# Optimization experiments

Hardware: AMD Instinct MI355X
Metric: run time of the kernel (lower is better)

Reference implementation:

```python
import jax, jax.numpy as jnp
import numpy as np

GN_GROUPS = 32
GN_EPS = 1e-5


def _conv3x3(x, w, b):
    # NCHW 3x3 conv, stride 1, pad 1
    y = jax.lax.conv_general_dilated(x, w, (1, 1), [(1, 1), (1, 1)],
                                     dimension_numbers=('NCHW', 'OIHW', 'NCHW'))
    return y + b[None, :, None, None]


def _bilinear(x, py, px):
    # x: [N,C,H,W]; py,px: [N,H,W] fractional sample coords; zeros outside.
    N, C, H, W = x.shape
    y0 = jnp.floor(py)
    x0 = jnp.floor(px)
    wy = py - y0
    wx = px - x0
    xf = x.reshape(N, C, H * W)
    out = jnp.zeros((N, C, H, W), x.dtype)
    corners = ((y0, x0, (1 - wy) * (1 - wx)),
               (y0, x0 + 1, (1 - wy) * wx),
               (y0 + 1, x0, wy * (1 - wx)),
               (y0 + 1, x0 + 1, wy * wx))
    for yy, xx, w in corners:
        valid = ((yy >= 0) & (yy <= H - 1) & (xx >= 0) & (xx <= W - 1)).astype(x.dtype)
        yi = jnp.clip(yy, 0, H - 1).astype(jnp.int32)
        xi = jnp.clip(xx, 0, W - 1).astype(jnp.int32)
        idx = (yi * W + xi).reshape(N, 1, H * W)
        g = jnp.take_along_axis(xf, idx, axis=2).reshape(N, C, H, W)
        out = out + g * (w * valid)[:, None]
    return out


def setup_inputs() -> dict:
    key = jax.random.key(0)
    ks = jax.random.split(key, 8)
    N, C, H, W = 4, 128, 160, 160
    s = 0.05
    return {
        'x': jax.random.normal(ks[0], (N, C, H, W), jnp.float32),
        'w_tm': jax.random.normal(ks[1], (4, C, 3, 3), jnp.float32) * s,
        'b_tm': jax.random.normal(ks[2], (4,), jnp.float32) * s,
        'w_tr': jax.random.normal(ks[3], (2, C, 3, 3), jnp.float32) * s,
        'b_tr': jax.random.normal(ks[4], (2,), jnp.float32) * s,
        'w_dcn': jax.random.normal(ks[5], (C, C, 3, 3), jnp.float32) * s,
        'gn_gamma': jnp.ones((C,), jnp.float32),
        'gn_beta': jnp.zeros((C,), jnp.float32),
    }


def reference(x, w_tm, b_tm, w_tr, b_tr, w_dcn, gn_gamma, gn_beta):
    N, C, H, W = x.shape
    Cout = w_dcn.shape[0]
    # regular 3x3 grid offsets: row0 = ky, row1 = kx, k ordered ky-major
    R = jnp.array([[-1., -1., -1., 0., 0., 0., 1., 1., 1.],
                   [-1., 0., 1., -1., 0., 1., -1., 0., 1.]], x.dtype)
    tm = _conv3x3(x, w_tm, b_tm)   # [N,4,H,W] -> per-pixel 2x2 affine
    tr = _conv3x3(x, w_tr, b_tr)   # [N,2,H,W] -> per-pixel (dy,dx) translation
    tmm = tm.transpose(0, 2, 3, 1).reshape(N, H, W, 2, 2)
    off = jnp.einsum('nhwij,jk->nhwik', tmm, R) - R  # [N,H,W,2,9]
    dy = off[:, :, :, 0, :] + tr[:, 0][..., None]    # [N,H,W,9]
    dx = off[:, :, :, 1, :] + tr[:, 1][..., None]
    hh = jnp.arange(H, dtype=x.dtype)[None, :, None, None]
    ww = jnp.arange(W, dtype=x.dtype)[None, None, :, None]
    kk = jnp.arange(9)
    ky = (kk // 3).astype(x.dtype)
    kx = (kk % 3).astype(x.dtype)
    py = hh - 1.0 + ky + dy  # stride=1, pad=1, dilation=1
    px = ww - 1.0 + kx + dx
    wk = w_dcn.reshape(Cout, C, 9)
    out = jnp.zeros((N, Cout, H, W), x.dtype)
    for k in range(9):  # fixed small loop over kernel points
        s = _bilinear(x, py[..., k], px[..., k])
        out = out + jnp.einsum('nchw,oc->nohw', s, wk[:, :, k])
    # GroupNorm
    og = out.reshape(N, GN_GROUPS, (Cout // GN_GROUPS) * H * W)
    mu = og.mean(axis=2, keepdims=True)
    var = og.var(axis=2, keepdims=True)
    og = (og - mu) * jax.lax.rsqrt(var + GN_EPS)
    out = og.reshape(N, Cout, H, W) * gn_gamma[None, :, None, None] + gn_beta[None, :, None, None]
    return jax.nn.relu(out + x)
```

## Files before the change

### kernel.cpp

```cpp
#include <hip/hip_runtime.h>
#include <hip/hip_fp16.h>
#include <math.h>

#define Hh 160
#define Ww 160
#define Cc 128
#define HW 25600
#define NPIX 102400

typedef __attribute__((ext_vector_type(8))) _Float16 half8;
typedef __attribute__((ext_vector_type(4))) float f32x4;
typedef __attribute__((ext_vector_type(4))) unsigned int u32x4;

union h2u { __half2 h; unsigned int u; };

#define WS_OFFS 0u
#define WS_WA   7372800u
#define WS_GSUM 7667712u
#define WS_GSQ  7668224u
#define WS_XT   7668736u
#define WS_RAW  33883136u

__global__ void wtrans_kernel(const float* __restrict__ w_dcn,
                              unsigned short* __restrict__ wA) {
    int idx = blockIdx.x * 256 + threadIdx.x;
    if (idx >= 9 * 128 * 128) return;
    int k = idx >> 14;
    int o = (idx >> 7) & 127;
    int c = idx & 127;
    wA[idx] = __half_as_ushort(__float2half(w_dcn[(o * 128 + c) * 9 + k]));
}

__global__ void __launch_bounds__(256) xpose_kernel(
    const float* __restrict__ x, unsigned short* __restrict__ xT) {
    __shared__ float L[128 * 65];
    int b = blockIdx.x;
    int n = b / 400;
    int px0 = (b - n * 400) * 64;
    int t = threadIdx.x;
    const float* xn = x + (size_t)n * Cc * HW + px0;
#pragma unroll
    for (int i = 0; i < 32; ++i) {
        int idx = i * 256 + t;
        int ch = idx >> 6;
        int pxl = idx & 63;
        L[ch * 65 + pxl] = xn[(size_t)ch * HW + pxl];
    }
    __syncthreads();
    unsigned short* dst = xT + ((size_t)n * HW + px0) * 128;
#pragma unroll
    for (int j = 0; j < 16; ++j) {
        int idx = j * 256 + t;
        int pxl = idx >> 6;
        int cp = idx & 63;
        h2u cv;
        cv.h = __floats2half2_rn(L[(2 * cp) * 65 + pxl],
                                 L[(2 * cp + 1) * 65 + pxl]);
        *(unsigned int*)(dst + (size_t)pxl * 128 + cp * 2) = cv.u;
    }
}

__global__ void __launch_bounds__(256) offs_kernel(
    const float* __restrict__ x, const float* __restrict__ w_tm,
    const float* __restrict__ b_tm, const float* __restrict__ w_tr,
    const float* __restrict__ b_tr, float* __restrict__ offs2) {
    __shared__ float wt[128 * 9 * 8];
    int t = threadIdx.x;
    for (int idx = t; idx < 6912; idx += 256) {
        int j = idx % 6;
        int rest = idx / 6;
        int tap = rest % 9;
        int c = rest / 9;
        float v = (j < 4) ? w_tm[(j * 128 + c) * 9 + tap]
                          : w_tr[((j - 4) * 128 + c) * 9 + tap];
        wt[rest * 8 + j] = v;
    }
    __syncthreads();
    int bid = blockIdx.x;
    int blk = (bid & 7) * 50 + (bid >> 3);
    int p = blk * 256 + t;
    int n = p / HW;
    int hw = p - n * HW;
    int h = hw / Ww;
    int w = hw - h * Ww;
    int addr[9];
    float msk[9];
#pragma unroll
    for (int tap = 0; tap < 9; ++tap) {
        int dy = tap / 3 - 1, dx = tap % 3 - 1;
        int yy = h + dy, xx = w + dx;
        bool v = (yy >= 0) && (yy < Hh) && (xx >= 0) && (xx < Ww);
        addr[tap] = v ? yy * Ww + xx : 0;
        msk[tap] = v ? 1.f : 0.f;
    }
    float a0 = 0, a1 = 0, a2 = 0, a3 = 0, a4 = 0, a5 = 0;
    const float* xn = x + n * Cc * HW;
#pragma unroll 2
    for (int c = 0; c < Cc; ++c) {
        const float* xc = xn + c * HW;
#pragma unroll
        for (int tap = 0; tap < 9; ++tap) {
            float v = msk[tap] * xc[addr[tap]];
            const float* wp = &wt[(c * 9 + tap) * 8];
            float4 w4 = *(const float4*)wp;
            float2 w2 = *(const float2*)(wp + 4);
            a0 += v * w4.x; a1 += v * w4.y; a2 += v * w4.z; a3 += v * w4.w;
            a4 += v * w2.x; a5 += v * w2.y;
        }
    }
    a0 += b_tm[0]; a1 += b_tm[1]; a2 += b_tm[2]; a3 += b_tm[3];
    a4 += b_tr[0]; a5 += b_tr[1];
#pragma unroll
    for (int k = 0; k < 9; ++k) {
        float r0 = (float)(k / 3) - 1.f;
        float r1 = (float)(k % 3) - 1.f;
        float2 st;
        st.x = (float)h + a0 * r0 + a1 * r1 + a4;
        st.y = (float)w + a2 * r0 + a3 * r1 + a5;
        *(float2*)(offs2 + ((size_t)k * NPIX + p) * 2) = st;
    }
}

__global__ void __launch_bounds__(256, 3) dcn2_kernel(
    const unsigned short* __restrict__ xT, const float* __restrict__ offs2,
    const unsigned short* __restrict__ wA, float* __restrict__ raw,
    float* __restrict__ gsum, float* __restrict__ gsq) {
    __shared__ __align__(16) unsigned short Bt[2 * 64 * 128];
    int t = threadIdx.x;
    int lane = t & 63;
    int wid = t >> 6;
    int wm = wid & 1, wn = wid >> 1;
    int quad = lane >> 4, l15 = lane & 15;
    int sub = lane >> 4;
    int s = lane & 15;

    int bid = blockIdx.x;
    int blk = (bid & 7) * 200 + (bid >> 3);
    int px0 = blk * 64;
    int n = px0 / HW;
    int hw0 = px0 - n * HW;
    const unsigned short* xb = xT + (size_t)n * HW * 128;
    const char* Ag = (const char*)wA;
    const float2* offv = (const float2*)offs2;
    int pbase = px0 + wid * 16 + sub;
    int sb = s << 3;

    f32x4 acc[4][2];
#pragma unroll
    for (int i = 0; i < 4; ++i)
#pragma unroll
        for (int j = 0; j < 2; ++j) acc[i][j] = (f32x4)0.f;

    float2 pc[4], pcn[4];
    u32x4 v00[2], v01[2], v10[2], v11[2];
    float w00[2], w01[2], w10[2], w11[2];

#define ISSUE(sl, r) do {                                                   \
    float py_ = pc[r].x, px_ = pc[r].y;                                     \
    float y0f_ = floorf(py_), x0f_ = floorf(px_);                           \
    float fy_ = py_ - y0f_, fx_ = px_ - x0f_;                               \
    int y0_ = (int)y0f_, xi0_ = (int)x0f_;                                  \
    int y1_ = y0_ + 1, xi1_ = xi0_ + 1;                                     \
    float wa_ = (1.f - fy_) * (1.f - fx_), wb_ = (1.f - fy_) * fx_;         \
    float wc_ = fy_ * (1.f - fx_), wd_ = fy_ * fx_;                         \
    bool vy0_ = (unsigned)y0_ < (unsigned)Hh;                               \
    bool vy1_ = (unsigned)y1_ < (unsigned)Hh;                               \
    bool vx0_ = (unsigned)xi0_ < (unsigned)Ww;                              \
    bool vx1_ = (unsigned)xi1_ < (unsigned)Ww;                              \
    w00[sl] = (vy0_ && vx0_) ? wa_ : 0.f;                                   \
    w01[sl] = (vy0_ && vx1_) ? wb_ : 0.f;                                   \
    w10[sl] = (vy1_ && vx0_) ? wc_ : 0.f;                                   \
    w11[sl] = (vy1_ && vx1_) ? wd_ : 0.f;                                   \
    int cy0_ = vy0_ ? y0_ : 0, cy1_ = vy1_ ? y1_ : 0;                       \
    int cx0_ = vx0_ ? xi0_ : 0, cx1_ = vx1_ ? xi1_ : 0;                     \
    v00[sl] = *(const u32x4*)(xb + ((size_t)(cy0_ * Ww + cx0_) << 7) + sb); \
    v01[sl] = *(const u32x4*)(xb + ((size_t)(cy0_ * Ww + cx1_) << 7) + sb); \
    v10[sl] = *(const u32x4*)(xb + ((size_t)(cy1_ * Ww + cx0_) << 7) + sb); \
    v11[sl] = *(const u32x4*)(xb + ((size_t)(cy1_ * Ww + cx1_) << 7) + sb); \
} while (0)

#define COMBINE(sl, r, bufbase) do {                                        \
    int p_ = wid * 16 + (r) * 4 + sub;                                      \
    __half2 W00_ = __float2half2_rn(w00[sl]);                               \
    __half2 W01_ = __float2half2_rn(w01[sl]);                               \
    __half2 W10_ = __float2half2_rn(w10[sl]);                               \
    __half2 W11_ = __float2half2_rn(w11[sl]);                               \
    u32x4 outv_;                                                            \
    _Pragma("unroll")                                                       \
    for (int e = 0; e < 4; ++e) {                                           \
        h2u a_, b_, c_, d_, o_;                                             \
        a_.u = v00[sl][e]; b_.u = v01[sl][e];                               \
        c_.u = v10[sl][e]; d_.u = v11[sl][e];                               \
        __half2 t_ = __hmul2(W11_, d_.h);                                   \
        t_ = __hfma2(W10_, c_.h, t_);                                       \
        t_ = __hfma2(W01_, b_.h, t_);                                       \
        t_ = __hfma2(W00_, a_.h, t_);                                       \
        o_.h = t_;                                                          \
        outv_[e] = o_.u;                                                    \
    }                                                                       \
    *(u32x4*)&Bt[(bufbase) + p_ * 128 + ((s ^ (p_ & 15)) << 3)] = outv_;    \
} while (0)

#define MQUAD(q) do {                                                       \
    half8 a0_, a1_, a2_, a3_, b0_, b1_;                                     \
    a0_ = *(const half8*)(Ag + ((size_t)(k * 128 + wm * 64 + 0 + l15) << 8) \
                          + (q) * 64 + quad * 16);                          \
    a1_ = *(const half8*)(Ag + ((size_t)(k * 128 + wm * 64 + 16 + l15) << 8)\
                          + (q) * 64 + quad * 16);                          \
    a2_ = *(const half8*)(Ag + ((size_t)(k * 128 + wm * 64 + 32 + l15) << 8)\
                          + (q) * 64 + quad * 16);                          \
    a3_ = *(const half8*)(Ag + ((size_t)(k * 128 + wm * 64 + 48 + l15) << 8)\
                          + (q) * 64 + quad * 16);                          \
    {                                                                       \
        int row0_ = wn * 32 + l15;                                          \
        int row1_ = wn * 32 + 16 + l15;                                     \
        int ur0_ = ((q) * 4 + quad) ^ (row0_ & 15);                         \
        int ur1_ = ((q) * 4 + quad) ^ (row1_ & 15);                         \
        b0_ = *(const half8*)&Bt[bufr + row0_ * 128 + ur0_ * 8];            \
        b1_ = *(const half8*)&Bt[bufr + row1_ * 128 + ur1_ * 8];            \
    }                                                                       \
    acc[0][0] = __builtin_amdgcn_mfma_f32_16x16x32_f16(a0_, b0_, acc[0][0], 0, 0, 0); \
    acc[0][1] = __builtin_amdgcn_mfma_f32_16x16x32_f16(a0_, b1_, acc[0][1], 0, 0, 0); \
    acc[1][0] = __builtin_amdgcn_mfma_f32_16x16x32_f16(a1_, b0_, acc[1][0], 0, 0, 0); \
    acc[1][1] = __builtin_amdgcn_mfma_f32_16x16x32_f16(a1_, b1_, acc[1][1], 0, 0, 0); \
    acc[2][0] = __builtin_amdgcn_mfma_f32_16x16x32_f16(a2_, b0_, acc[2][0], 0, 0, 0); \
    acc[2][1] = __builtin_amdgcn_mfma_f32_16x16x32_f16(a2_, b1_, acc[2][1], 0, 0, 0); \
    acc[3][0] = __builtin_amdgcn_mfma_f32_16x16x32_f16(a3_, b0_, acc[3][0], 0, 0, 0); \
    acc[3][1] = __builtin_amdgcn_mfma_f32_16x16x32_f16(a3_, b1_, acc[3][1], 0, 0, 0); \
} while (0)

#pragma unroll
    for (int r = 0; r < 4; ++r) pc[r] = offv[pbase + r * 4];
    ISSUE(0, 0); ISSUE(1, 1);
    COMBINE(0, 0, 0); COMBINE(1, 1, 0);
    ISSUE(0, 2); ISSUE(1, 3);
    COMBINE(0, 2, 0); COMBINE(1, 3, 0);
#pragma unroll
    for (int r = 0; r < 4; ++r) pc[r] = offv[(size_t)1 * NPIX + pbase + r * 4];
    __syncthreads();

    for (int k = 0; k < 9; ++k) {
        int bufr = (k & 1) * (64 * 128);
        int bufw = ((k + 1) & 1) * (64 * 128);
        if (k < 7) {
#pragma unroll
            for (int r = 0; r < 4; ++r)
                pcn[r] = offv[(size_t)(k + 2) * NPIX + pbase + r * 4];
        }
        if (k < 8) { ISSUE(0, 0); ISSUE(1, 1); }
        MQUAD(0); MQUAD(1);
        if (k < 8) {
            COMBINE(0, 0, bufw); COMBINE(1, 1, bufw);
            ISSUE(0, 2); ISSUE(1, 3);
        }
        MQUAD(2); MQUAD(3);
        if (k < 8) { COMBINE(0, 2, bufw); COMBINE(1, 3, bufw); }
        __syncthreads();
        if (k < 7) {
#pragma unroll
            for (int r = 0; r < 4; ++r) pc[r] = pcn[r];
        }
    }

#undef ISSUE
#undef COMBINE
#undef MQUAD

    size_t rbase = ((size_t)n * Cc) * HW + hw0;
#pragma unroll
    for (int i = 0; i < 4; ++i) {
        float s_i = 0.f, q_i = 0.f;
#pragma unroll
        for (int j = 0; j < 2; ++j) {
            int pxl = wn * 32 + j * 16 + l15;
#pragma unroll
            for (int rr = 0; rr < 4; ++rr) {
                int o = wm * 64 + i * 16 + quad * 4 + rr;
                float v = acc[i][j][rr];
                raw[rbase + (size_t)o * HW + pxl] = v;
                s_i += v;
                q_i += v * v;
            }
        }
#pragma unroll
        for (int m = 1; m < 16; m <<= 1) {
            s_i += __shfl_xor(s_i, m);
            q_i += __shfl_xor(q_i, m);
        }
        if (l15 == 0) {
            int g = wm * 16 + i * 4 + quad;
            atomicAdd(&gsum[n * 32 + g], s_i);
            atomicAdd(&gsq[n * 32 + g], q_i);
        }
    }
}

__global__ void __launch_bounds__(256) finish_kernel(
    const float* __restrict__ raw, const float* __restrict__ x,
    const float* __restrict__ gsum, const float* __restrict__ gsq,
    const float* __restrict__ gamma, const float* __restrict__ beta,
    float* __restrict__ out) {
    int i = blockIdx.x * 256 + threadIdx.x;
    int e = i * 4;
    int n = e / (Cc * HW);
    int rem = e - n * (Cc * HW);
    int c = rem / HW;
    int g = c >> 2;
    const float inv = 1.f / 102400.f;
    float mu = gsum[n * 32 + g] * inv;
    float var = gsq[n * 32 + g] * inv - mu * mu;
    float rs = rsqrtf(var + 1e-5f);
    float sc = gamma[c] * rs;
    float sh = beta[c] - mu * sc;
    float4 v = *(const float4*)&raw[e];
    float4 xv = *(const float4*)&x[e];
    float4 r;
    r.x = fmaxf(v.x * sc + sh + xv.x, 0.f);
    r.y = fmaxf(v.y * sc + sh + xv.y, 0.f);
    r.z = fmaxf(v.z * sc + sh + xv.z, 0.f);
    r.w = fmaxf(v.w * sc + sh + xv.w, 0.f);
    *(float4*)&out[e] = r;
}

extern "C" void kernel_launch(void* const* d_in, const int* in_sizes, int n_in,
                              void* d_out, int out_size, void* d_ws, size_t ws_size,
                              hipStream_t stream) {
    const float* x      = (const float*)d_in[0];
    const float* w_tm   = (const float*)d_in[1];
    const float* b_tm   = (const float*)d_in[2];
    const float* w_tr   = (const float*)d_in[3];
    const float* b_tr   = (const float*)d_in[4];
    const float* w_dcn  = (const float*)d_in[5];
    const float* gamma  = (const float*)d_in[6];
    const float* beta   = (const float*)d_in[7];
    char* ws = (char*)d_ws;
    float*          offs2 = (float*)(ws + WS_OFFS);
    unsigned short* wA    = (unsigned short*)(ws + WS_WA);
    float*          gsum  = (float*)(ws + WS_GSUM);
    float*          gsq   = (float*)(ws + WS_GSQ);
    unsigned short* xT    = (unsigned short*)(ws + WS_XT);
    float*          raw   = (float*)(ws + WS_RAW);
    float* out = (float*)d_out;

    (void)hipMemsetAsync(gsum, 0, 1024, stream);
    wtrans_kernel<<<576, 256, 0, stream>>>(w_dcn, wA);
    xpose_kernel<<<1600, 256, 0, stream>>>(x, xT);
    offs_kernel<<<400, 256, 0, stream>>>(x, w_tm, b_tm, w_tr, b_tr, offs2);
    dcn2_kernel<<<1600, 256, 0, stream>>>(xT, offs2, wA, raw, gsum, gsq);
    finish_kernel<<<12800, 256, 0, stream>>>(raw, x, gsum, gsq, gamma, beta, out);
}
```

Before: 400.8 us.

## Drop LDS double buffering in DCN kernel and raise occupancy to 4 blocks

Replaces the software-pipelined double-buffered LDS scheme, where bilinear gathers for the next tap overlapped MFMA on the current tap, with a single LDS buffer. Each tap now gathers and combines first, syncs, then runs the MFMAs, with two barriers per tap. LDS use is halved and launch bounds rise to 4 blocks per SM, so latency is meant to be hidden by more resident waves rather than by explicit in-block overlap. The cost is losing the intra-block overlap of gather and MFMA, plus an extra barrier per tap.

```diff
diff --git a/kernel.cpp b/kernel.cpp
--- a/kernel.cpp
+++ b/kernel.cpp
@@ -121,11 +121,11 @@
     }
 }
 
-__global__ void __launch_bounds__(256, 3) dcn2_kernel(
+__global__ void __launch_bounds__(256, 4) dcn2_kernel(
     const unsigned short* __restrict__ xT, const float* __restrict__ offs2,
     const unsigned short* __restrict__ wA, float* __restrict__ raw,
     float* __restrict__ gsum, float* __restrict__ gsq) {
-    __shared__ __align__(16) unsigned short Bt[2 * 64 * 128];
+    __shared__ __align__(16) unsigned short Bt[64 * 128];
     int t = threadIdx.x;
     int lane = t & 63;
     int wid = t >> 6;
@@ -179,7 +179,7 @@
     v11[sl] = *(const u32x4*)(xb + ((size_t)(cy1_ * Ww + cx1_) << 7) + sb); \
 } while (0)
 
-#define COMBINE(sl, r, bufbase) do {                                        \
+#define COMBINE(sl, r) do {                                                 \
     int p_ = wid * 16 + (r) * 4 + sub;                                      \
     __half2 W00_ = __float2half2_rn(w00[sl]);                               \
     __half2 W01_ = __float2half2_rn(w01[sl]);                               \
@@ -198,65 +198,50 @@
         o_.h = t_;                                                          \
         outv_[e] = o_.u;                                                    \
     }                                                                       \
-    *(u32x4*)&Bt[(bufbase) + p_ * 128 + ((s ^ (p_ & 15)) << 3)] = outv_;    \
+    *(u32x4*)&Bt[p_ * 128 + ((s ^ (p_ & 15)) << 3)] = outv_;                \
 } while (0)
 
-#define MQUAD(q) do {                                                       \
-    half8 a0_, a1_, a2_, a3_, b0_, b1_;                                     \
-    a0_ = *(const half8*)(Ag + ((size_t)(k * 128 + wm * 64 + 0 + l15) << 8) \
-                          + (q) * 64 + quad * 16);                          \
-    a1_ = *(const half8*)(Ag + ((size_t)(k * 128 + wm * 64 + 16 + l15) << 8)\
-                          + (q) * 64 + quad * 16);                          \
-    a2_ = *(const half8*)(Ag + ((size_t)(k * 128 + wm * 64 + 32 + l15) << 8)\
-                          + (q) * 64 + quad * 16);                          \
-    a3_ = *(const half8*)(Ag + ((size_t)(k * 128 + wm * 64 + 48 + l15) << 8)\
-                          + (q) * 64 + quad * 16);                          \
-    {                                                                       \
-        int row0_ = wn * 32 + l15;                                          \
-        int row1_ = wn * 32 + 16 + l15;                                     \
-        int ur0_ = ((q) * 4 + quad) ^ (row0_ & 15);                         \
-        int ur1_ = ((q) * 4 + quad) ^ (row1_ & 15);                         \
-        b0_ = *(const half8*)&Bt[bufr + row0_ * 128 + ur0_ * 8];            \
-        b1_ = *(const half8*)&Bt[bufr + row1_ * 128 + ur1_ * 8];            \
-    }                                                                       \
-    acc[0][0] = __builtin_amdgcn_mfma_f32_16x16x32_f16(a0_, b0_, acc[0][0], 0, 0, 0); \
-    acc[0][1] = __builtin_amdgcn_mfma_f32_16x16x32_f16(a0_, b1_, acc[0][1], 0, 0, 0); \
-    acc[1][0] = __builtin_amdgcn_mfma_f32_16x16x32_f16(a1_, b0_, acc[1][0], 0, 0, 0); \
-    acc[1][1] = __builtin_amdgcn_mfma_f32_16x16x32_f16(a1_, b1_, acc[1][1], 0, 0, 0); \
-    acc[2][0] = __builtin_amdgcn_mfma_f32_16x16x32_f16(a2_, b0_, acc[2][0], 0, 0, 0); \
-    acc[2][1] = __builtin_amdgcn_mfma_f32_16x16x32_f16(a2_, b1_, acc[2][1], 0, 0, 0); \
-    acc[3][0] = __builtin_amdgcn_mfma_f32_16x16x32_f16(a3_, b0_, acc[3][0], 0, 0, 0); \
-    acc[3][1] = __builtin_amdgcn_mfma_f32_16x16x32_f16(a3_, b1_, acc[3][1], 0, 0, 0); \
-} while (0)
-
 #pragma unroll
     for (int r = 0; r < 4; ++r) pc[r] = offv[pbase + r * 4];
-    ISSUE(0, 0); ISSUE(1, 1);
-    COMBINE(0, 0, 0); COMBINE(1, 1, 0);
-    ISSUE(0, 2); ISSUE(1, 3);
-    COMBINE(0, 2, 0); COMBINE(1, 3, 0);
-#pragma unroll
-    for (int r = 0; r < 4; ++r) pc[r] = offv[(size_t)1 * NPIX + pbase + r * 4];
-    __syncthreads();
 
     for (int k = 0; k < 9; ++k) {
-        int bufr = (k & 1) * (64 * 128);
-        int bufw = ((k + 1) & 1) * (64 * 128);
-        if (k < 7) {
+        __syncthreads();
+
+        if (k < 8) {
 #pragma unroll
             for (int r = 0; r < 4; ++r)
-                pcn[r] = offv[(size_t)(k + 2) * NPIX + pbase + r * 4];
-        }
-        if (k < 8) { ISSUE(0, 0); ISSUE(1, 1); }
-        MQUAD(0); MQUAD(1);
+                pcn[r] = offv[(size_t)(k + 1) * NPIX + pbase + r * 4];
+        }
+
+        ISSUE(0, 0); ISSUE(1, 1);
+        COMBINE(0, 0); COMBINE(1, 1);
+        ISSUE(0, 2); ISSUE(1, 3);
+        COMBINE(0, 2); COMBINE(1, 3);
+        __syncthreads();
+
+#pragma unroll
+        for (int q = 0; q < 4; ++q) {
+            half8 a[4], b[2];
+#pragma unroll
+            for (int i = 0; i < 4; ++i)
+                a[i] = *(const half8*)(Ag +
+                        ((size_t)(k * 128 + wm * 64 + i * 16 + l15) << 8) +
+                        q * 64 + quad * 16);
+#pragma unroll
+            for (int j = 0; j < 2; ++j) {
+                int row = wn * 32 + j * 16 + l15;
+                int ur = (q * 4 + quad) ^ (row & 15);
+                b[j] = *(const half8*)&Bt[row * 128 + ur * 8];
+            }
+#pragma unroll
+            for (int i = 0; i < 4; ++i)
+#pragma unroll
+                for (int j = 0; j < 2; ++j)
+                    acc[i][j] = __builtin_amdgcn_mfma_f32_16x16x32_f16(
+                        a[i], b[j], acc[i][j], 0, 0, 0);
+        }
+
         if (k < 8) {
-            COMBINE(0, 0, bufw); COMBINE(1, 1, bufw);
-            ISSUE(0, 2); ISSUE(1, 3);
-        }
-        MQUAD(2); MQUAD(3);
-        if (k < 8) { COMBINE(0, 2, bufw); COMBINE(1, 3, bufw); }
-        __syncthreads();
-        if (k < 7) {
 #pragma unroll
             for (int r = 0; r < 4; ++r) pc[r] = pcn[r];
         }
@@ -264,7 +249,6 @@
 
 #undef ISSUE
 #undef COMBINE
-#undef MQUAD
 
     size_t rbase = ((size_t)n * Cc) * HW + hw0;
 #pragma unroll
```

Measured after the change: 389.4 us. -2.8%, faster.
